# Kernel optimization log

Hardware: AMD Instinct MI355X
Metric: run time of the kernel (lower is better)

## Reference

```python
import jax, jax.numpy as jnp
import numpy as np

B, N, F_IN, F_HID, F_OUT = 32, 1024, 512, 512, 512


def setup_inputs() -> dict:
    key = jax.random.key(0)
    ks = jax.random.split(key, 8)
    def xavier(k, fan_in, fan_out):
        bound = float(np.sqrt(6.0 / (fan_in + fan_out)))
        return jax.random.uniform(k, (fan_in, fan_out), jnp.float32, -bound, bound)
    return {
        "batch_graph": jax.random.normal(ks[0], (B, N, F_IN), jnp.float32),
        "adj": jax.random.uniform(ks[1], (B, N, N), jnp.float32),
        "W1": xavier(ks[2], F_IN, F_HID),
        "b1": jnp.zeros((F_HID,), jnp.float32),
        "W2": xavier(ks[3], F_HID, F_HID),
        "b2": jnp.zeros((F_HID,), jnp.float32),
        "W3": xavier(ks[4], F_HID, F_OUT),
        "b3": jnp.zeros((F_OUT,), jnp.float32),
    }


def _gcn_layer(x, adj, W, b):
    # support = X @ W ; out = A @ support + b  (per graph in the batch)
    support = jnp.einsum("bnf,fh->bnh", x, W)
    return jnp.einsum("bnm,bmh->bnh", adj, support) + b


def reference(batch_graph, adj, W1, b1, W2, b2, W3, b3):
    # Block-diagonal big_adj @ big_graph is exactly a batched per-graph matmul:
    # the zero off-diagonal blocks contribute nothing, so math is identical.
    # Dropout is identity at inference (eval mode).
    x = jax.nn.relu(_gcn_layer(batch_graph, adj, W1, b1))
    x = jax.nn.relu(_gcn_layer(x, adj, W2, b2))
    out = _gcn_layer(x, adj, W3, b3)  # [B, N, F_OUT]
    return out
```

## Files before the change

### kernel.cpp

```cpp
#include <hip/hip_runtime.h>
#include <hip/hip_bf16.h>


typedef __attribute__((ext_vector_type(8))) short bf16x8s;
typedef __attribute__((ext_vector_type(4))) float f32x4;
typedef __attribute__((ext_vector_type(4))) unsigned short us4;
typedef __attribute__((ext_vector_type(8))) unsigned short us8;

__device__ __forceinline__ unsigned short f2bf(float f) {
    unsigned u = __builtin_bit_cast(unsigned, f);
    u += 0x7fffu + ((u >> 16) & 1u);
    return (unsigned short)(u >> 16);
}

__device__ __forceinline__ void async16(const unsigned short* g, unsigned short* l) {
    __builtin_amdgcn_global_load_lds(
        (const __attribute__((address_space(1))) unsigned int*)g,
        (__attribute__((address_space(3))) unsigned int*)l, 16, 0, 0);
}

#define MFMA_(d, va, vb) d = __builtin_amdgcn_mfma_f32_16x16x32_bf16(va, vb, d, 0, 0, 0)

__global__ void cvt_f32_bf16(const float* __restrict__ in, unsigned short* __restrict__ out, long n4) {
    long i = (long)blockIdx.x * blockDim.x + threadIdx.x;
    long stride = (long)gridDim.x * blockDim.x;
    for (; i < n4; i += stride) {
        float4 v = ((const float4*)in)[i];
        us4 o;
        o.x = f2bf(v.x); o.y = f2bf(v.y); o.z = f2bf(v.z); o.w = f2bf(v.w);
        ((us4*)out)[i] = o;
    }
}

__global__ void transpose_cvt(const float* __restrict__ W, unsigned short* __restrict__ WT,
                              int R, int C) {
    int idx = blockIdx.x * 256 + threadIdx.x;
    if (idx >= R * C) return;
    int r = idx % R;
    int c = idx / R;
    WT[(size_t)c * R + r] = f2bf(W[(size_t)r * C + c]);
}

template<bool RELU, bool OUT_F32>
__global__ __launch_bounds__(512, 2)
void gemm256(const unsigned short* __restrict__ A,
             const unsigned short* __restrict__ BT,
             void* __restrict__ Cout,
             const float* __restrict__ bias,
             int M, int N, int K,
             long sA, long sBT, long sC)
{
    __shared__ unsigned short Lraw[65536];

    const int t    = threadIdx.x;
    const int lane = t & 63;
    const int wv   = t >> 6;
    const int wm   = wv >> 2;
    const int wn   = wv & 3;
    const int fr   = lane & 15;
    const int fk   = (lane >> 4) * 8;
    const int r4   = (lane >> 4) * 4;

    const int tilesN = N >> 8;
    const int bpb    = (M >> 8) * tilesN;
    const int cpx = gridDim.x >> 3;
    const int lb  = (blockIdx.x & 7) * cpx + (blockIdx.x >> 3);
    const int bat = lb / bpb;
    const int tt  = lb % bpb;
    const int m0  = (tt / tilesN) << 8;
    const int n0  = (tt % tilesN) << 8;

    const unsigned short* Ab = A  + (size_t)bat * sA  + (size_t)m0 * K;
    const unsigned short* Bb = BT + (size_t)bat * sBT + (size_t)n0 * K;

    int srow[2], scol[2], lo[2];
#pragma unroll
    for (int r = 0; r < 2; ++r) {
        int c   = r * 512 + t;
        srow[r] = c >> 3;
        scol[r] = ((c & 7) * 8) ^ ((srow[r] & 7) << 3);
        lo[r]   = c * 8;
    }

    auto stageA = [&](int kt, int h) {
        unsigned short* base = Lraw + (kt & 1) * 16384;
#pragma unroll
        for (int r = 0; r < 2; ++r)
            async16(Ab + (size_t)(h * 128 + srow[r]) * K + kt * 64 + scol[r],
                    base + h * 8192 + lo[r]);
    };
    auto stageB = [&](int kt, int h) {
        unsigned short* base = Lraw + 32768 + (kt & 1) * 16384;
#pragma unroll
        for (int r = 0; r < 2; ++r)
            async16(Bb + (size_t)(h * 128 + srow[r]) * K + kt * 64 + scol[r],
                    base + h * 8192 + lo[r]);
    };
    auto rdA = [&](int buf, int mf, int kkj) -> bf16x8s {
        int row = wm * 128 + mf * 16 + fr;
        int e   = (kkj * 32 + fk) ^ ((row & 7) << 3);
        return *(const bf16x8s*)&Lraw[buf * 16384 + row * 64 + e];
    };
    auto rdB = [&](int buf, int nf, int kkj) -> bf16x8s {
        int row = wn * 64 + nf * 16 + fr;
        int e   = (kkj * 32 + fk) ^ ((row & 7) << 3);
        return *(const bf16x8s*)&Lraw[32768 + buf * 16384 + row * 64 + e];
    };

    const int nt = K >> 6;

    f32x4 acc[8][4];
#pragma unroll
    for (int i = 0; i < 8; ++i)
#pragma unroll
        for (int j = 0; j < 4; ++j) acc[i][j] = f32x4{0.f, 0.f, 0.f, 0.f};

    stageA(0, 0); stageA(0, 1); stageB(0, 0); stageB(0, 1);
    if (nt > 1) {
        stageB(1, 0); stageB(1, 1);
        asm volatile("s_waitcnt vmcnt(4)" ::: "memory");
    } else {
        asm volatile("s_waitcnt vmcnt(0)" ::: "memory");
    }
    __builtin_amdgcn_s_barrier();

    bf16x8s bfr[4][2];
    for (int it = 0; it < nt; ++it) {
        const int cur = it & 1;
        bf16x8s a0, a1, a2, a3;

#pragma unroll
        for (int nf = 0; nf < 4; ++nf) {
            bfr[nf][0] = rdB(cur, nf, 0);
            bfr[nf][1] = rdB(cur, nf, 1);
        }
        a0 = rdA(cur, 0, 0); a1 = rdA(cur, 0, 1);
        a2 = rdA(cur, 1, 0); a3 = rdA(cur, 1, 1);
        if (it + 1 < nt) stageA(it + 1, 0);
        __builtin_amdgcn_s_barrier();
        asm volatile("s_waitcnt lgkmcnt(0)" ::: "memory");
        __builtin_amdgcn_sched_barrier(0);
        __builtin_amdgcn_s_setprio(1);
#pragma unroll
        for (int nf = 0; nf < 4; ++nf) {
            MFMA_(acc[0][nf], a0, bfr[nf][0]);
            MFMA_(acc[0][nf], a1, bfr[nf][1]);
            MFMA_(acc[1][nf], a2, bfr[nf][0]);
            MFMA_(acc[1][nf], a3, bfr[nf][1]);
        }
        __builtin_amdgcn_s_setprio(0);
        __builtin_amdgcn_s_barrier();

        a0 = rdA(cur, 2, 0); a1 = rdA(cur, 2, 1);
        a2 = rdA(cur, 3, 0); a3 = rdA(cur, 3, 1);
        if (it + 1 < nt) stageA(it + 1, 1);
        __builtin_amdgcn_s_barrier();
        asm volatile("s_waitcnt lgkmcnt(0)" ::: "memory");
        __builtin_amdgcn_sched_barrier(0);
        __builtin_amdgcn_s_setprio(1);
#pragma unroll
        for (int nf = 0; nf < 4; ++nf) {
            MFMA_(acc[2][nf], a0, bfr[nf][0]);
            MFMA_(acc[2][nf], a1, bfr[nf][1]);
            MFMA_(acc[3][nf], a2, bfr[nf][0]);
            MFMA_(acc[3][nf], a3, bfr[nf][1]);
        }
        __builtin_amdgcn_s_setprio(0);
        __builtin_amdgcn_s_barrier();

        a0 = rdA(cur, 4, 0); a1 = rdA(cur, 4, 1);
        a2 = rdA(cur, 5, 0); a3 = rdA(cur, 5, 1);
        if (it + 2 < nt) stageB(it + 2, 0);
        __builtin_amdgcn_s_barrier();
        asm volatile("s_waitcnt lgkmcnt(0)" ::: "memory");
        __builtin_amdgcn_sched_barrier(0);
        __builtin_amdgcn_s_setprio(1);
#pragma unroll
        for (int nf = 0; nf < 4; ++nf) {
            MFMA_(acc[4][nf], a0, bfr[nf][0]);
            MFMA_(acc[4][nf], a1, bfr[nf][1]);
            MFMA_(acc[5][nf], a2, bfr[nf][0]);
            MFMA_(acc[5][nf], a3, bfr[nf][1]);
        }
        __builtin_amdgcn_s_setprio(0);
        __builtin_amdgcn_s_barrier();

        a0 = rdA(cur, 6, 0); a1 = rdA(cur, 6, 1);
        a2 = rdA(cur, 7, 0); a3 = rdA(cur, 7, 1);
        if (it + 2 < nt) stageB(it + 2, 1);
        __builtin_amdgcn_s_barrier();
        asm volatile("s_waitcnt lgkmcnt(0)" ::: "memory");
        __builtin_amdgcn_sched_barrier(0);
        __builtin_amdgcn_s_setprio(1);
#pragma unroll
        for (int nf = 0; nf < 4; ++nf) {
            MFMA_(acc[6][nf], a0, bfr[nf][0]);
            MFMA_(acc[6][nf], a1, bfr[nf][1]);
            MFMA_(acc[7][nf], a2, bfr[nf][0]);
            MFMA_(acc[7][nf], a3, bfr[nf][1]);
        }
        __builtin_amdgcn_s_setprio(0);
        if (it < nt - 2)       asm volatile("s_waitcnt vmcnt(4)" ::: "memory");
        else if (it == nt - 2) asm volatile("s_waitcnt vmcnt(0)" ::: "memory");
        __builtin_amdgcn_s_barrier();
    }

    const int R0 = m0 + wm * 128;
    const int C0 = n0 + wn * 64;
    float bv[4];
#pragma unroll
    for (int j = 0; j < 4; ++j)
        bv[j] = bias ? bias[C0 + j * 16 + fr] : 0.f;

    if (OUT_F32) {
        float* Cb = (float*)Cout + (size_t)bat * sC;
#pragma unroll
        for (int j = 0; j < 4; ++j)
#pragma unroll
            for (int i = 0; i < 8; ++i)
#pragma unroll
                for (int e = 0; e < 4; ++e) {
                    float v = acc[i][j][e] + bv[j];
                    if (RELU) v = fmaxf(v, 0.f);
                    Cb[(size_t)(R0 + i * 16 + r4 + e) * N + C0 + j * 16 + fr] = v;
                }
    } else {
        unsigned short* sl = Lraw + wv * 8192;
#pragma unroll
        for (int i = 0; i < 8; ++i)
#pragma unroll
            for (int j = 0; j < 4; ++j)
#pragma unroll
                for (int e = 0; e < 4; ++e) {
                    float v = acc[i][j][e] + bv[j];
                    if (RELU) v = fmaxf(v, 0.f);
                    const int row = i * 16 + r4 + e;
                    const int col = j * 16 + fr;
                    sl[row * 64 + (col ^ ((row & 7) << 3))] = f2bf(v);
                }
        unsigned short* Cb = (unsigned short*)Cout + (size_t)bat * sC;
#pragma unroll
        for (int rr = 0; rr < 16; ++rr) {
            const int row = rr * 8 + (lane >> 3);
            const int k8  = lane & 7;
            us8 v = *(const us8*)&sl[row * 64 + ((k8 ^ (row & 7)) << 3)];
            *(us8*)&Cb[(size_t)(R0 + row) * N + C0 + k8 * 8] = v;
        }
    }
}

extern "C" void kernel_launch(void* const* d_in, const int* in_sizes, int n_in,
                              void* d_out, int out_size, void* d_ws, size_t ws_size,
                              hipStream_t stream) {
    constexpr int B = 32, N = 1024, F = 512;

    const float* x0f  = (const float*)d_in[0];
    const float* adjf = (const float*)d_in[1];
    const float* W1 = (const float*)d_in[2];
    const float* b1 = (const float*)d_in[3];
    const float* W2 = (const float*)d_in[4];
    const float* b2 = (const float*)d_in[5];
    const float* W3 = (const float*)d_in[6];
    const float* b3 = (const float*)d_in[7];

    unsigned short* ws   = (unsigned short*)d_ws;
    unsigned short* adjb = ws;
    unsigned short* P0   = adjb + (size_t)B * N * N;
    unsigned short* P1   = P0 + (size_t)B * N * F;
    unsigned short* PT   = P1 + (size_t)B * N * F;
    unsigned short* WT1  = PT + (size_t)B * N * F;
    unsigned short* WT2  = WT1 + (size_t)F * F;
    unsigned short* WT3  = WT2 + (size_t)F * F;

    cvt_f32_bf16<<<2048, 256, 0, stream>>>(adjf, adjb, (long)B * N * N / 4);
    cvt_f32_bf16<<<2048, 256, 0, stream>>>(x0f, P0, (long)B * N * F / 4);
    transpose_cvt<<<(F * F) / 256, 256, 0, stream>>>(W1, WT1, F, F);
    transpose_cvt<<<(F * F) / 256, 256, 0, stream>>>(W2, WT2, F, F);
    transpose_cvt<<<(F * F) / 256, 256, 0, stream>>>(W3, WT3, F, F);

    const int grid = 256;
    const long sX = (long)N * F;
    const long sAd = (long)N * N;

    gemm256<false, false><<<grid, 512, 0, stream>>>(WT1,  P0, PT, nullptr, F, N, F, 0,  sX, sX);
    gemm256<true,  false><<<grid, 512, 0, stream>>>(adjb, PT, P1, b1,      N, F, N, sAd, sX, sX);
    gemm256<false, false><<<grid, 512, 0, stream>>>(WT2,  P1, PT, nullptr, F, N, F, 0,  sX, sX);
    gemm256<true,  false><<<grid, 512, 0, stream>>>(adjb, PT, P0, b2,      N, F, N, sAd, sX, sX);
    gemm256<false, false><<<grid, 512, 0, stream>>>(WT3,  P0, PT, nullptr, F, N, F, 0,  sX, sX);
    gemm256<false, true ><<<grid, 512, 0, stream>>>(adjb, PT, (float*)d_out, b3, N, F, N, sAd, sX, sX);
}
```

Baseline: 269.9 us.

## Restructure GEMM main loop into quadrant MFMA schedule and fuse prep kernels

Replaces the per-iteration schedule, which issued eight A/B load-then-MFMA phases, with four quadrant phases. Each phase runs 16 MFMAs while the next A/B fragments are read from LDS and the next k-tile's global-to-LDS loads are in flight. It reads B fragments in halves and waits for all outstanding loads (vmcnt(0)) before each tile, so prefetch depth drops from two B tiles ahead to one tile. It also merges the x0 conversion and the three weight transpose-convert launches into one prep kernel to cut launch overhead. Risks are less latency hiding from the shallower prefetch and a possible LDS read-write race on the shared buffer.

Measured after the change: 256.3 us. -5.1%, faster.

```diff
diff --git a/kernel.cpp b/kernel.cpp
--- a/kernel.cpp
+++ b/kernel.cpp
@@ -20,6 +20,31 @@
 }
 
 #define MFMA_(d, va, vb) d = __builtin_amdgcn_mfma_f32_16x16x32_bf16(va, vb, d, 0, 0, 0)
+
+__global__ void prep(const float* __restrict__ x0, unsigned short* __restrict__ P0, long n4,
+                     const float* __restrict__ W1, const float* __restrict__ W2,
+                     const float* __restrict__ W3, unsigned short* __restrict__ WT1,
+                     unsigned short* __restrict__ WT2, unsigned short* __restrict__ WT3,
+                     int F) {
+    long i = (long)blockIdx.x * blockDim.x + threadIdx.x;
+    long stride = (long)gridDim.x * blockDim.x;
+    for (long k = i; k < n4; k += stride) {
+        float4 v = ((const float4*)x0)[k];
+        us4 o;
+        o.x = f2bf(v.x); o.y = f2bf(v.y); o.z = f2bf(v.z); o.w = f2bf(v.w);
+        ((us4*)P0)[k] = o;
+    }
+    const long FF = (long)F * F;
+    for (long k = i; k < 3 * FF; k += stride) {
+        int w = (int)(k / FF);
+        long idx = k % FF;
+        int r = (int)(idx % F);
+        int c = (int)(idx / F);
+        const float* W = (w == 0) ? W1 : (w == 1) ? W2 : W3;
+        unsigned short* WT = (w == 0) ? WT1 : (w == 1) ? WT2 : WT3;
+        WT[idx] = f2bf(W[(size_t)r * F + c]);
+    }
+}
 
 __global__ void cvt_f32_bf16(const float* __restrict__ in, unsigned short* __restrict__ out, long n4) {
     long i = (long)blockIdx.x * blockDim.x + threadIdx.x;
@@ -30,15 +55,6 @@
         o.x = f2bf(v.x); o.y = f2bf(v.y); o.z = f2bf(v.z); o.w = f2bf(v.w);
         ((us4*)out)[i] = o;
     }
-}
-
-__global__ void transpose_cvt(const float* __restrict__ W, unsigned short* __restrict__ WT,
-                              int R, int C) {
-    int idx = blockIdx.x * 256 + threadIdx.x;
-    if (idx >= R * C) return;
-    int r = idx % R;
-    int c = idx / R;
-    WT[(size_t)c * R + r] = f2bf(W[(size_t)r * C + c]);
 }
 
 template<bool RELU, bool OUT_F32>
@@ -115,95 +131,72 @@
 #pragma unroll
         for (int j = 0; j < 4; ++j) acc[i][j] = f32x4{0.f, 0.f, 0.f, 0.f};
 
-    stageA(0, 0); stageA(0, 1); stageB(0, 0); stageB(0, 1);
-    if (nt > 1) {
-        stageB(1, 0); stageB(1, 1);
-        asm volatile("s_waitcnt vmcnt(4)" ::: "memory");
-    } else {
-        asm volatile("s_waitcnt vmcnt(0)" ::: "memory");
-    }
+    bf16x8s aP[4], aB[4], aC[4], bX[4], bY[4];
+
+    stageA(0, 0); stageB(0, 0); stageA(0, 1); stageB(0, 1);
+    asm volatile("s_waitcnt vmcnt(0)" ::: "memory");
     __builtin_amdgcn_s_barrier();
-
-    bf16x8s bfr[4][2];
+#pragma unroll
+    for (int m = 0; m < 4; ++m) aP[m] = rdA(0, m, 0);
+#pragma unroll
+    for (int n = 0; n < 4; ++n) bX[n] = rdB(0, n, 0);
+
     for (int it = 0; it < nt; ++it) {
-        const int cur = it & 1;
-        bf16x8s a0, a1, a2, a3;
-
-#pragma unroll
-        for (int nf = 0; nf < 4; ++nf) {
-            bfr[nf][0] = rdB(cur, nf, 0);
-            bfr[nf][1] = rdB(cur, nf, 1);
+        const int cur  = it & 1;
+        const int nxt  = cur ^ 1;
+        const bool more = (it + 1 < nt);
+
+        __builtin_amdgcn_s_barrier();
+#pragma unroll
+        for (int m = 0; m < 4; ++m) aB[m] = rdA(cur, m + 4, 0);
+        if (more) { stageA(it + 1, 0); stageB(it + 1, 0); }
+        __builtin_amdgcn_s_setprio(1);
+#pragma unroll
+        for (int m = 0; m < 4; ++m)
+#pragma unroll
+            for (int n = 0; n < 4; ++n) MFMA_(acc[m][n], aP[m], bX[n]);
+        __builtin_amdgcn_s_setprio(0);
+
+        __builtin_amdgcn_s_barrier();
+#pragma unroll
+        for (int m = 0; m < 4; ++m) aC[m] = rdA(cur, m, 1);
+#pragma unroll
+        for (int n = 0; n < 4; ++n) bY[n] = rdB(cur, n, 1);
+        if (more) { stageA(it + 1, 1); stageB(it + 1, 1); }
+        __builtin_amdgcn_s_setprio(1);
+#pragma unroll
+        for (int m = 0; m < 4; ++m)
+#pragma unroll
+            for (int n = 0; n < 4; ++n) MFMA_(acc[m + 4][n], aB[m], bX[n]);
+        __builtin_amdgcn_s_setprio(0);
+
+        __builtin_amdgcn_s_barrier();
+#pragma unroll
+        for (int m = 0; m < 4; ++m) aB[m] = rdA(cur, m + 4, 1);
+        __builtin_amdgcn_s_setprio(1);
+#pragma unroll
+        for (int m = 0; m < 4; ++m)
+#pragma unroll
+            for (int n = 0; n < 4; ++n) MFMA_(acc[m][n], aC[m], bY[n]);
+        __builtin_amdgcn_s_setprio(0);
+
+        if (more) {
+            asm volatile("s_waitcnt vmcnt(0)" ::: "memory");
+            __builtin_amdgcn_s_barrier();
+#pragma unroll
+            for (int m = 0; m < 4; ++m) aP[m] = rdA(nxt, m, 0);
+#pragma unroll
+            for (int n = 0; n < 4; ++n) bX[n] = rdB(nxt, n, 0);
         }
-        a0 = rdA(cur, 0, 0); a1 = rdA(cur, 0, 1);
-        a2 = rdA(cur, 1, 0); a3 = rdA(cur, 1, 1);
-        if (it + 1 < nt) stageA(it + 1, 0);
-        __builtin_amdgcn_s_barrier();
-        asm volatile("s_waitcnt lgkmcnt(0)" ::: "memory");
-        __builtin_amdgcn_sched_barrier(0);
-        __builtin_amdgcn_s_setprio(1);
-#pragma unroll
-        for (int nf = 0; nf < 4; ++nf) {
-            MFMA_(acc[0][nf], a0, bfr[nf][0]);
-            MFMA_(acc[0][nf], a1, bfr[nf][1]);
-            MFMA_(acc[1][nf], a2, bfr[nf][0]);
-            MFMA_(acc[1][nf], a3, bfr[nf][1]);
-        }
-        __builtin_amdgcn_s_setprio(0);
-        __builtin_amdgcn_s_barrier();
-
-        a0 = rdA(cur, 2, 0); a1 = rdA(cur, 2, 1);
-        a2 = rdA(cur, 3, 0); a3 = rdA(cur, 3, 1);
-        if (it + 1 < nt) stageA(it + 1, 1);
-        __builtin_amdgcn_s_barrier();
-        asm volatile("s_waitcnt lgkmcnt(0)" ::: "memory");
-        __builtin_amdgcn_sched_barrier(0);
-        __builtin_amdgcn_s_setprio(1);
-#pragma unroll
-        for (int nf = 0; nf < 4; ++nf) {
-            MFMA_(acc[2][nf], a0, bfr[nf][0]);
-            MFMA_(acc[2][nf], a1, bfr[nf][1]);
-            MFMA_(acc[3][nf], a2, bfr[nf][0]);
-            MFMA_(acc[3][nf], a3, bfr[nf][1]);
-        }
-        __builtin_amdgcn_s_setprio(0);
-        __builtin_amdgcn_s_barrier();
-
-        a0 = rdA(cur, 4, 0); a1 = rdA(cur, 4, 1);
-        a2 = rdA(cur, 5, 0); a3 = rdA(cur, 5, 1);
-        if (it + 2 < nt) stageB(it + 2, 0);
-        __builtin_amdgcn_s_barrier();
-        asm volatile("s_waitcnt lgkmcnt(0)" ::: "memory");
-        __builtin_amdgcn_sched_barrier(0);
-        __builtin_amdgcn_s_setprio(1);
-#pragma unroll
-        for (int nf = 0; nf < 4; ++nf) {
-            MFMA_(acc[4][nf], a0, bfr[nf][0]);
-            MFMA_(acc[4][nf], a1, bfr[nf][1]);
-            MFMA_(acc[5][nf], a2, bfr[nf][0]);
-            MFMA_(acc[5][nf], a3, bfr[nf][1]);
-        }
-        __builtin_amdgcn_s_setprio(0);
-        __builtin_amdgcn_s_barrier();
-
-        a0 = rdA(cur, 6, 0); a1 = rdA(cur, 6, 1);
-        a2 = rdA(cur, 7, 0); a3 = rdA(cur, 7, 1);
-        if (it + 2 < nt) stageB(it + 2, 1);
-        __builtin_amdgcn_s_barrier();
-        asm volatile("s_waitcnt lgkmcnt(0)" ::: "memory");
-        __builtin_amdgcn_sched_barrier(0);
-        __builtin_amdgcn_s_setprio(1);
-#pragma unroll
-        for (int nf = 0; nf < 4; ++nf) {
-            MFMA_(acc[6][nf], a0, bfr[nf][0]);
-            MFMA_(acc[6][nf], a1, bfr[nf][1]);
-            MFMA_(acc[7][nf], a2, bfr[nf][0]);
-            MFMA_(acc[7][nf], a3, bfr[nf][1]);
-        }
-        __builtin_amdgcn_s_setprio(0);
-        if (it < nt - 2)       asm volatile("s_waitcnt vmcnt(4)" ::: "memory");
-        else if (it == nt - 2) asm volatile("s_waitcnt vmcnt(0)" ::: "memory");
-        __builtin_amdgcn_s_barrier();
-    }
+        __builtin_amdgcn_s_setprio(1);
+#pragma unroll
+        for (int m = 0; m < 4; ++m)
+#pragma unroll
+            for (int n = 0; n < 4; ++n) MFMA_(acc[m + 4][n], aB[m], bY[n]);
+        __builtin_amdgcn_s_setprio(0);
+    }
+
+    __syncthreads();
 
     const int R0 = m0 + wm * 128;
     const int C0 = n0 + wn * 64;
@@ -272,11 +265,9 @@
     unsigned short* WT2  = WT1 + (size_t)F * F;
     unsigned short* WT3  = WT2 + (size_t)F * F;
 
+    prep<<<2048, 256, 0, stream>>>(x0f, P0, (long)B * N * F / 4,
+                                   W1, W2, W3, WT1, WT2, WT3, F);
     cvt_f32_bf16<<<2048, 256, 0, stream>>>(adjf, adjb, (long)B * N * N / 4);
-    cvt_f32_bf16<<<2048, 256, 0, stream>>>(x0f, P0, (long)B * N * F / 4);
-    transpose_cvt<<<(F * F) / 256, 256, 0, stream>>>(W1, WT1, F, F);
-    transpose_cvt<<<(F * F) / 256, 256, 0, stream>>>(W2, WT2, F, F);
-    transpose_cvt<<<(F * F) / 256, 256, 0, stream>>>(W3, WT3, F, F);
 
     const int grid = 256;
     const long sX = (long)N * F;
```
